# Optimization experiments

Hardware: AMD Instinct MI355X
Metric: run time of the kernel (lower is better)

Reference implementation:

```python
import jax, jax.numpy as jnp
import numpy as np

EPS = 1e-5


def conv2d(x, w, b, pad, mode='reflect'):
    # x: [B,C,H,W], w: [O,I,kh,kw]
    if pad > 0:
        x = jnp.pad(x, ((0, 0), (0, 0), (pad, pad), (pad, pad)), mode=mode)
    y = jax.lax.conv_general_dilated(x, w, (1, 1), 'VALID',
                                     dimension_numbers=('NCHW', 'OIHW', 'NCHW'))
    return y + b[None, :, None, None]


def inorm(x):
    # InstanceNorm2d, no affine (nn.InstanceNorm2d default)
    m = jnp.mean(x, axis=(2, 3), keepdims=True)
    v = jnp.mean((x - m) ** 2, axis=(2, 3), keepdims=True)
    return (x - m) * jax.lax.rsqrt(v + EPS)


def upsample2(x):
    # nn.Upsample(scale_factor=2), default nearest
    return jnp.repeat(jnp.repeat(x, 2, axis=2), 2, axis=3)


def bilinear_sample(img, py, px):
    # img [B,C,H,W]; py/px [B,H,W] float coords; zero padding outside bounds
    B, C, H, W = img.shape
    y0 = jnp.floor(py)
    x0 = jnp.floor(px)
    wy1 = (py - y0)[:, None]
    wx1 = (px - x0)[:, None]
    wy0 = 1.0 - wy1
    wx0 = 1.0 - wx1
    y0i = y0.astype(jnp.int32)
    x0i = x0.astype(jnp.int32)
    flat = img.reshape(B, C, H * W)

    def tap(yi, xi):
        valid = (yi >= 0) & (yi < H) & (xi >= 0) & (xi < W)
        idx = jnp.clip(yi, 0, H - 1) * W + jnp.clip(xi, 0, W - 1)
        g = jnp.take_along_axis(flat, idx.reshape(B, 1, H * W), axis=2).reshape(B, C, H, W)
        return g * valid[:, None]

    return (tap(y0i, x0i) * wy0 * wx0 + tap(y0i, x0i + 1) * wy0 * wx1 +
            tap(y0i + 1, x0i) * wy1 * wx0 + tap(y0i + 1, x0i + 1) * wy1 * wx1)


def mdcn(x, offset, mask, w, b):
    # modulated deformable conv v2: 3x3, stride 1, pad 1, 1 deformable group
    # offset [B,18,H,W] read as interleaved (dy,dx) per kernel tap; mask [B,9,H,W]
    B, C, H, W = x.shape
    off = offset.reshape(B, 9, 2, H, W)
    base_y = jnp.arange(H, dtype=x.dtype)[None, :, None]
    base_x = jnp.arange(W, dtype=x.dtype)[None, None, :]
    cols = []
    for k in range(9):
        ky, kx = k // 3 - 1, k % 3 - 1
        py = base_y + ky + off[:, k, 0]
        px = base_x + kx + off[:, k, 1]
        cols.append(bilinear_sample(x, py, px) * mask[:, k][:, None])
    col = jnp.stack(cols, axis=2)  # [B,C,9,H,W]
    out = jnp.einsum('bckhw,ock->bohw', col, w.reshape(w.shape[0], C, 9))
    return out + b[None, :, None, None]


def dcn_block(out, skip, off_w, off_b, w, b):
    # ModulatedDeformConvPack(double=True): offsets from concat, deform conv on skip
    dc = jnp.concatenate([out, skip], axis=1)
    om = conv2d(dc, off_w, off_b, 1, mode='constant')
    o1, o2, m = jnp.split(om, 3, axis=1)
    offset = jnp.concatenate([o1, o2], axis=1)
    pre = mdcn(skip, offset, jax.nn.sigmoid(m), w, b)
    return jnp.concatenate([pre, out], axis=1), offset


def decoder_fwd(x, skip1, skip2,
                rb0_w1, rb0_b1, rb0_w2, rb0_b2,
                rb1_w1, rb1_b1, rb1_w2, rb1_b2,
                conv1_w, conv1_b, conv3_w, conv3_b,
                conv5_w, conv5_b, conv6_w, conv6_b,
                dcn2_off_w, dcn2_off_b, dcn2_w, dcn2_b,
                dcn1_off_w, dcn1_off_b, dcn1_w, dcn1_b):
    out = x
    # i=0: ResBlocks (2 resblocks, 'in' norm, relu, reflect pad)
    for (w1, b1, w2, b2) in ((rb0_w1, rb0_b1, rb0_w2, rb0_b2),
                             (rb1_w1, rb1_b1, rb1_w2, rb1_b2)):
        h = jax.nn.relu(inorm(conv2d(out, w1, b1, 1)))
        out = out + inorm(conv2d(h, w2, b2, 1))
    # i=1: Conv2dBlock(256->256, 5x5)
    out = jax.nn.relu(inorm(conv2d(out, conv1_w, conv1_b, 2)))
    # dcn_2 hook (baseline_idx=2 -> dcn_idx=[1,3])
    out, offset2 = dcn_block(out, skip2, dcn2_off_w, dcn2_off_b, dcn2_w, dcn2_b)
    # i=2: upsample
    out = upsample2(out)
    # i=3: Conv2dBlock(512->128, 5x5)
    out = jax.nn.relu(inorm(conv2d(out, conv3_w, conv3_b, 2)))
    # dcn hook
    out, offset1 = dcn_block(out, skip1, dcn1_off_w, dcn1_off_b, dcn1_w, dcn1_b)
    # i=4: upsample
    out = upsample2(out)
    # i=5: Conv2dBlock(256->64, 5x5)
    out = jax.nn.relu(inorm(conv2d(out, conv5_w, conv5_b, 2)))
    # i=6: Conv2dBlock(64->3, 7x7, no norm, tanh)
    out = jnp.tanh(conv2d(out, conv6_w, conv6_b, 3))
    offset_sum = 0.5 * (jnp.mean(jnp.abs(offset1)) + jnp.mean(jnp.abs(offset2)))
    return out, offset_sum


def setup_inputs() -> dict:
    key = jax.random.key(0)
    ks = iter(jax.random.split(key, 48))

    def randn(shape, scale=1.0):
        return jax.random.normal(next(ks), shape, dtype=jnp.float32) * scale

    def conv_w(o, i, k, scale=1.0):
        return randn((o, i, k, k), scale / float(np.sqrt(i * k * k)))

    d = {}
    d['x'] = randn((8, 256, 32, 32))
    d['skip1'] = randn((8, 128, 64, 64))
    d['skip2'] = randn((8, 256, 32, 32))
    for r in range(2):
        d[f'rb{r}_w1'] = conv_w(256, 256, 3)
        d[f'rb{r}_b1'] = randn((256,), 0.01)
        d[f'rb{r}_w2'] = conv_w(256, 256, 3)
        d[f'rb{r}_b2'] = randn((256,), 0.01)
    d['conv1_w'] = conv_w(256, 256, 5); d['conv1_b'] = randn((256,), 0.01)
    d['conv3_w'] = conv_w(128, 512, 5); d['conv3_b'] = randn((128,), 0.01)
    d['conv5_w'] = conv_w(64, 256, 5); d['conv5_b'] = randn((64,), 0.01)
    d['conv6_w'] = conv_w(3, 64, 7); d['conv6_b'] = randn((3,), 0.01)
    d['dcn2_off_w'] = conv_w(27, 512, 3, 0.1); d['dcn2_off_b'] = randn((27,), 0.01)
    d['dcn2_w'] = conv_w(256, 256, 3); d['dcn2_b'] = randn((256,), 0.01)
    d['dcn1_off_w'] = conv_w(27, 256, 3, 0.1); d['dcn1_off_b'] = randn((27,), 0.01)
    d['dcn1_w'] = conv_w(128, 128, 3); d['dcn1_b'] = randn((128,), 0.01)
    return d


def reference(x, skip1, skip2,
              rb0_w1, rb0_b1, rb0_w2, rb0_b2,
              rb1_w1, rb1_b1, rb1_w2, rb1_b2,
              conv1_w, conv1_b, conv3_w, conv3_b,
              conv5_w, conv5_b, conv6_w, conv6_b,
              dcn2_off_w, dcn2_off_b, dcn2_w, dcn2_b,
              dcn1_off_w, dcn1_off_b, dcn1_w, dcn1_b):
    return decoder_fwd(x, skip1, skip2,
                       rb0_w1, rb0_b1, rb0_w2, rb0_b2,
                       rb1_w1, rb1_b1, rb1_w2, rb1_b2,
                       conv1_w, conv1_b, conv3_w, conv3_b,
                       conv5_w, conv5_b, conv6_w, conv6_b,
                       dcn2_off_w, dcn2_off_b, dcn2_w, dcn2_b,
                       dcn1_off_w, dcn1_off_b, dcn1_w, dcn1_b)
```

## Files before the change

kernel.cpp:

```cpp
#include <hip/hip_runtime.h>
#include <hip/hip_bf16.h>
#include <math.h>

typedef __hip_bfloat16 bf16;
typedef unsigned short u16;
typedef __attribute__((ext_vector_type(8))) short short8;
typedef __attribute__((ext_vector_type(4))) float f32x4;

__device__ __forceinline__ float LD(const float* p) { return *p; }
__device__ __forceinline__ float LD(const bf16* p)  { return __bfloat162float(*p); }
__device__ __forceinline__ void  ST(float* p, float v) { *p = v; }
__device__ __forceinline__ void  ST(bf16* p, float v)  { *p = __float2bfloat16(v); }
__device__ __forceinline__ u16   f2b(float v) { bf16 h = __float2bfloat16(v); return *reinterpret_cast<u16*>(&h); }
__device__ __forceinline__ float b2fu(u16 u) { bf16 h = *reinterpret_cast<bf16*>(&u); return __bfloat162float(h); }

__global__ __launch_bounds__(256) void copy_kernel(const float* __restrict__ in,
                                                   float* __restrict__ out, int n) {
    int i = blockIdx.x * blockDim.x + threadIdx.x;
    if (i < n) out[i] = in[i];
}

__global__ __launch_bounds__(256) void wsplit_kernel(const float* __restrict__ w,
                                                     u16* __restrict__ hi, u16* __restrict__ lo,
                                                     int O, int C, int KK)
{
    const int i = blockIdx.x * 256 + threadIdx.x;
    const int n = O * C * KK;
    if (i >= n) return;
    const int o = i / (C * KK);
    const int r = i - o * C * KK;
    const int c = r / KK;
    const int t = r - c * KK;
    const float v = w[i];
    const bf16 h = __float2bfloat16(v);
    const float hv = __bfloat162float(h);
    const bf16 l = __float2bfloat16(v - hv);
    const size_t dst = ((size_t)t * O + o) * C + c;
    hi[dst] = *(const u16*)&h;
    lo[dst] = *(const u16*)&l;
}

__global__ __launch_bounds__(256) void wsplit2_kernel(const float* __restrict__ w,
                                                      u16* __restrict__ hi, u16* __restrict__ lo,
                                                      int O, int C, int KK)
{
    const int i = blockIdx.x * 256 + threadIdx.x;
    const int n = O * C * KK;
    if (i >= n) return;
    const int o = i / (C * KK);
    const int r = i - o * C * KK;
    const int c = r / KK;
    const int t = r - c * KK;
    const float v = w[i];
    const bf16 h = __float2bfloat16(v);
    const float hv = __bfloat162float(h);
    const bf16 l = __float2bfloat16(v - hv);
    const int nch = C >> 5;
    const int cc = c >> 5, quad = (c >> 3) & 3, q = c & 7;
    const size_t dst = ((((size_t)t * nch + cc) * 4 + quad) * O + o) * 8 + q;
    hi[dst] = *(const u16*)&h;
    lo[dst] = *(const u16*)&l;
}

__global__ __launch_bounds__(256) void wsplitL_kernel(const float* __restrict__ w,
        u16* __restrict__ lh, u16* __restrict__ ll, u16* __restrict__ ch, int O, int C)
{
    const int i = blockIdx.x * 256 + threadIdx.x;
    const int n = O * C * 50;
    if (i >= n) return;
    const int s = i / (O * C);
    const int r = i - s * (O * C);
    const int o = r / C;
    const int c = r - o * C;
    const size_t U = (size_t)C * O;
    const int cc = c >> 5, quad = (c >> 3) & 3, q = c & 7;
    const size_t din = (((size_t)cc * 4 + quad) * O + o) * 8 + q;
    const float* wp = w + ((size_t)o * C + c) * 25;
    if (s < 30) {
        const int ry = s / 15, rem = s % 15, j = rem / 5, tx = rem % 5;
        int ys, yn;
        if (ry == 0) { ys = (j == 0) ? 0 : (j == 1) ? 2 : 4; yn = (j == 2) ? 1 : 2; }
        else         { ys = (j == 0) ? 0 : (j == 1) ? 1 : 3; yn = (j == 0) ? 1 : 2; }
        float v = 0.f;
        for (int ty = ys; ty < ys + yn; ++ty) v += wp[ty * 5 + tx];
        const bf16 h = __float2bfloat16(v);
        const bf16 l = __float2bfloat16(v - __bfloat162float(h));
        lh[(size_t)s * U + din] = *(const u16*)&h;
        ll[(size_t)s * U + din] = *(const u16*)&l;
    } else {
        const int t = s - 30;
        const int cidx = t / 5, tx = t - cidx * 5;
        const int tyc = (cidx == 0) ? 0 : (cidx == 1) ? 1 : (cidx == 2) ? 3 : 4;
        const bf16 h = __float2bfloat16(wp[tyc * 5 + tx]);
        ch[(size_t)t * U + din] = *(const u16*)&h;
    }
}

template<typename T1, typename T2, int K, bool UP, int EPI, bool ASPLIT,
         int NR, int NCOL, int MT, int MW>
__global__ __launch_bounds__(MW * 128) void conv_mfma3(
        const T1* __restrict__ src1, const T2* __restrict__ src2,
        int C1, int C,
        const u16* __restrict__ wth, const u16* __restrict__ wtl,
        const float* __restrict__ bias,
        void* __restrict__ outv, int O, int H, int W)
{
    constexpr int KK = K * K;
    constexpr int ATILE = NR * NCOL * 32;
    __shared__ __align__(16) u16 Ah[ATILE];
    __shared__ __align__(16) u16 Al[ASPLIT ? ATILE : 8];

    const int tid  = threadIdx.x;
    const int lane = tid & 63;
    const int wv   = tid >> 6;
    const int ln15 = lane & 15;
    const int quad = lane >> 4;
    const int mi = wv % MW, ni = wv / MW;
    const int b = blockIdx.y;
    const int p0 = blockIdx.x * (MT * 16 * MW);
    const int obase = blockIdx.z * 64;
    const int HW = H * W;
    const int SH = UP ? (H >> 1) : H;
    const int SW = UP ? (W >> 1) : W;
    const int SHW = SH * SW;
    const int PAD = K / 2;
    const int C2 = C - C1;
    const int nch = C >> 5;

    const int y0 = p0 / W;
    const int rbase = (y0 <= PAD) ? 0 : (UP ? ((y0 - PAD) >> 1) : (y0 - PAD));

    int rs[MT][K], cs[MT][K];
#pragma unroll
    for (int ms = 0; ms < MT; ++ms) {
        const int pm = p0 + mi * (MT * 16) + ms * 16 + ln15;
        const int ym = pm / W, xm = pm - ym * W;
#pragma unroll
        for (int tt = 0; tt < K; ++tt) {
            int yy = ym + tt - PAD;
            yy = yy < 0 ? -yy : yy; yy = yy >= H ? 2 * H - 2 - yy : yy;
            rs[ms][tt] = (UP ? (yy >> 1) : yy) - rbase;
            int xx = xm + tt - PAD;
            xx = xx < 0 ? -xx : xx; xx = xx >= W ? 2 * W - 2 - xx : xx;
            cs[ms][tt] = UP ? (xx >> 1) : xx;
        }
    }

    f32x4 acc[MT][2];
#pragma unroll
    for (int i = 0; i < MT; ++i)
#pragma unroll
        for (int j = 0; j < 2; ++j) acc[i][j] = (f32x4)0.f;

    for (int cc = 0; cc < nch; ++cc) {
        const int c0 = cc << 5;
        __syncthreads();
        for (int idx = tid; idx < NR * NCOL * 4; idx += MW * 128) {
            const int c_ = idx % NCOL;
            const int r_ = (idx / NCOL) % NR;
            const int cq = idx / (NCOL * NR);
            int rr = rbase + r_; rr = rr >= SH ? SH - 1 : rr;
            const int sidx = rr * SW + c_;
            short8 vh, vl;
#pragma unroll
            for (int q = 0; q < 8; ++q) {
                const int c = c0 + cq * 8 + q;
                float v;
                if (c < C1) v = LD(src1 + (size_t)(b * C1 + c) * SHW + sidx);
                else        v = LD(src2 + (size_t)(b * C2 + (c - C1)) * SHW + sidx);
                const u16 hv = f2b(v);
                vh[q] = (short)hv;
                if (ASPLIT) vl[q] = (short)f2b(v - b2fu(hv));
            }
            *(short8*)&Ah[idx * 8] = vh;
            if (ASPLIT) *(short8*)&Al[idx * 8] = vl;
        }
        __syncthreads();

#pragma unroll
        for (int t = 0; t < KK; ++t) {
            const int ty = t / K, tx = t - ty * K;
            const size_t wb0 = ((((size_t)t * nch + cc) * 4 + quad) * O
                                + obase + ni * 32 + ln15) * 8;
            const short8 b0h = *(const short8*)(wth + wb0);
            const short8 b1h = *(const short8*)(wth + wb0 + 128);
            const short8 b0l = *(const short8*)(wtl + wb0);
            const short8 b1l = *(const short8*)(wtl + wb0 + 128);
#pragma unroll
            for (int ms = 0; ms < MT; ++ms) {
                const int ao = ((quad * NR + rs[ms][ty]) * NCOL + cs[ms][tx]) * 8;
                const short8 a = *(const short8*)&Ah[ao];
                acc[ms][0] = __builtin_amdgcn_mfma_f32_16x16x32_bf16(a, b0h, acc[ms][0], 0, 0, 0);
                acc[ms][0] = __builtin_amdgcn_mfma_f32_16x16x32_bf16(a, b0l, acc[ms][0], 0, 0, 0);
                acc[ms][1] = __builtin_amdgcn_mfma_f32_16x16x32_bf16(a, b1h, acc[ms][1], 0, 0, 0);
                acc[ms][1] = __builtin_amdgcn_mfma_f32_16x16x32_bf16(a, b1l, acc[ms][1], 0, 0, 0);
                if (ASPLIT) {
                    const short8 al = *(const short8*)&Al[ao];
                    acc[ms][0] = __builtin_amdgcn_mfma_f32_16x16x32_bf16(al, b0h, acc[ms][0], 0, 0, 0);
                    acc[ms][1] = __builtin_amdgcn_mfma_f32_16x16x32_bf16(al, b1h, acc[ms][1], 0, 0, 0);
                }
            }
        }
    }

#pragma unroll
    for (int ms = 0; ms < MT; ++ms) {
#pragma unroll
        for (int ns = 0; ns < 2; ++ns) {
            const int o = obase + ni * 32 + ns * 16 + ln15;
            const float bv = bias[o];
            const f32x4 av = acc[ms][ns];
#pragma unroll
            for (int r = 0; r < 4; ++r) {
                const int pp = p0 + mi * (MT * 16) + ms * 16 + (quad << 2) + r;
                const float v = av[r] + bv;
                const size_t oidx = ((size_t)(b * O + o)) * HW + pp;
                if (EPI == 0) ((float*)outv)[oidx] = v;
                else          ((bf16*)outv)[oidx] = __float2bfloat16(v);
            }
        }
    }
}

template<typename T1, typename T2, int NR, int NCOL, int MT, int MW>
__global__ __launch_bounds__(MW * 128) void conv_mfma5(
        const T1* __restrict__ src1, const T2* __restrict__ src2,
        int C1, int C,
        const u16* __restrict__ wLh, const u16* __restrict__ wLl,
        const u16* __restrict__ wCh,
        const float* __restrict__ bias,
        bf16* __restrict__ out, int O, int H, int W)
{
    constexpr int NRR = NR + 1;
    __shared__ __align__(16) u16 Ah[4 * NRR * NCOL * 8];

    const int tid  = threadIdx.x;
    const int lane = tid & 63;
    const int wv   = tid >> 6;
    const int ln15 = lane & 15;
    const int quad = lane >> 4;
    const int mi = wv % MW, ni = wv / MW;
    const int b = blockIdx.y;
    const int p0 = blockIdx.x * (MT * 16 * MW);
    const int obase = blockIdx.z * 64;
    const int HW = H * W;
    const int SH = H >> 1, SW = W >> 1;
    const int SHW = SH * SW;
    const int C2 = C - C1;
    const int nch = C >> 5;
    const size_t U = (size_t)C * O;

    const int y0 = p0 / W;
    const int rbase = (y0 <= 2) ? 0 : ((y0 - 2) >> 1);

    const int ym0 = (p0 + mi * (MT * 16)) / W;
    const int ry = ym0 & 1;
    const int uu = ym0 >> 1;
    int r0 = uu - 1, r2 = uu + 1;
    r0 = r0 < 0 ? 1 : r0;
    r2 = r2 >= SH ? SH - 2 : r2;
    const int rg0 = r0 - rbase, rg1 = uu - rbase, rg2 = r2 - rbase;

    const bool isTopW = (ym0 <= 1), isBotW = (ym0 >= H - 2);
    const bool isBorderW = isTopW || isBotW;
    int cidx = 0;
    if (isTopW) cidx = (ym0 == 0) ? 1 : 0;
    if (isBotW) cidx = (ym0 == H - 2) ? 3 : 2;
    const bool blkTop = (p0 == 0);
    const bool blkBot = (p0 + MW * MT * 16 == HW);
    const bool blkEdge = blkTop || blkBot;

    int cs[MT][5];
#pragma unroll
    for (int ms = 0; ms < MT; ++ms) {
        const int pm = p0 + mi * (MT * 16) + ms * 16 + ln15;
        const int xm = pm % W;
#pragma unroll
        for (int tt = 0; tt < 5; ++tt) {
            int xx = xm + tt - 2;
            xx = xx < 0 ? -xx : xx; xx = xx >= W ? 2 * W - 2 - xx : xx;
            cs[ms][tt] = xx >> 1;
        }
    }

    f32x4 acc[MT][2];
#pragma unroll
    for (int i = 0; i < MT; ++i)
#pragma unroll
        for (int j = 0; j < 2; ++j) acc[i][j] = (f32x4)0.f;

    for (int cc = 0; cc < nch; ++cc) {
        const int c0 = cc << 5;
        __syncthreads();
        for (int idx = tid; idx < NR * NCOL * 4; idx += MW * 128) {
            const int c_ = idx % NCOL;
            const int r_ = (idx / NCOL) % NR;
            const int cq = idx / (NCOL * NR);
            int rr = rbase + r_; rr = rr >= SH ? SH - 1 : rr;
            const int sidx = rr * SW + c_;
            short8 vh;
#pragma unroll
            for (int q = 0; q < 8; ++q) {
                const int c = c0 + cq * 8 + q;
                float v;
                if (c < C1) v = LD(src1 + (size_t)(b * C1 + c) * SHW + sidx);
                else        v = LD(src2 + (size_t)(b * C2 + (c - C1)) * SHW + sidx);
                vh[q] = (short)f2b(v);
            }
            *(short8*)&Ah[((cq * NRR + r_) * NCOL + c_) * 8] = vh;
        }
        if (blkEdge) {
            const int ra = blkTop ? 0 : SH - 1;
            const int rb2 = blkTop ? 1 : SH - 2;
            for (int idx = tid; idx < NCOL * 4; idx += MW * 128) {
                const int c_ = idx % NCOL;
                const int cq = idx / NCOL;
                short8 vh;
#pragma unroll
                for (int q = 0; q < 8; ++q) {
                    const int c = c0 + cq * 8 + q;
                    float va, vb;
                    if (c < C1) {
                        const size_t base = (size_t)(b * C1 + c) * SHW;
                        va = LD(src1 + base + ra * SW + c_);
                        vb = LD(src1 + base + rb2 * SW + c_);
                    } else {
                        const size_t base = (size_t)(b * C2 + (c - C1)) * SHW;
                        va = LD(src2 + base + ra * SW + c_);
                        vb = LD(src2 + base + rb2 * SW + c_);
                    }
                    vh[q] = (short)f2b(va - vb);
                }
                *(short8*)&Ah[((cq * NRR + NR) * NCOL + c_) * 8] = vh;
            }
        }
        __syncthreads();

        const size_t wq = ((size_t)(cc * 4 + quad) * O + obase + ni * 32 + ln15) * 8;
#pragma unroll
        for (int j = 0; j < 3; ++j) {
            const int rgj = (j == 0) ? rg0 : (j == 1) ? rg1 : rg2;
#pragma unroll
            for (int tx = 0; tx < 5; ++tx) {
                const size_t wb = (size_t)((ry * 3 + j) * 5 + tx) * U + wq;
                const short8 b0h = *(const short8*)(wLh + wb);
                const short8 b1h = *(const short8*)(wLh + wb + 128);
                const short8 b0l = *(const short8*)(wLl + wb);
                const short8 b1l = *(const short8*)(wLl + wb + 128);
#pragma unroll
                for (int ms = 0; ms < MT; ++ms) {
                    const int ao = ((quad * NRR + rgj) * NCOL + cs[ms][tx]) * 8;
                    const short8 a = *(const short8*)&Ah[ao];
                    acc[ms][0] = __builtin_amdgcn_mfma_f32_16x16x32_bf16(a, b0h, acc[ms][0], 0, 0, 0);
                    acc[ms][0] = __builtin_amdgcn_mfma_f32_16x16x32_bf16(a, b0l, acc[ms][0], 0, 0, 0);
                    acc[ms][1] = __builtin_amdgcn_mfma_f32_16x16x32_bf16(a, b1h, acc[ms][1], 0, 0, 0);
                    acc[ms][1] = __builtin_amdgcn_mfma_f32_16x16x32_bf16(a, b1l, acc[ms][1], 0, 0, 0);
                }
            }
        }
        if (isBorderW) {
#pragma unroll
            for (int tx = 0; tx < 5; ++tx) {
                const size_t wb = (size_t)(cidx * 5 + tx) * U + wq;
                const short8 b0 = *(const short8*)(wCh + wb);
                const short8 b1 = *(const short8*)(wCh + wb + 128);
#pragma unroll
                for (int ms = 0; ms < MT; ++ms) {
                    const int ao = ((quad * NRR + NR) * NCOL + cs[ms][tx]) * 8;
                    const short8 a = *(const short8*)&Ah[ao];
                    acc[ms][0] = __builtin_amdgcn_mfma_f32_16x16x32_bf16(a, b0, acc[ms][0], 0, 0, 0);
                    acc[ms][1] = __builtin_amdgcn_mfma_f32_16x16x32_bf16(a, b1, acc[ms][1], 0, 0, 0);
                }
            }
        }
    }

#pragma unroll
    for (int ms = 0; ms < MT; ++ms) {
#pragma unroll
        for (int ns = 0; ns < 2; ++ns) {
            const int o = obase + ni * 32 + ns * 16 + ln15;
            const float bv = bias[o];
            const f32x4 av = acc[ms][ns];
#pragma unroll
            for (int r = 0; r < 4; ++r) {
                const int pp = p0 + mi * (MT * 16) + ms * 16 + (quad << 2) + r;
                out[((size_t)(b * O + o)) * HW + pp] = __float2bfloat16(av[r] + bv);
            }
        }
    }
}

template<typename OT, bool ASPLIT>
__global__ __launch_bounds__(256) void mdcn_mfma(
        const float* __restrict__ skip, const float* __restrict__ om,
        const u16* __restrict__ wth, const u16* __restrict__ wtl,
        const float* __restrict__ bias,
        OT* __restrict__ out, int C, int O, int H, int W)
{
    __shared__ float tpy[576], tpxs[576], tms[576];
    __shared__ __align__(16) u16 Ah[2][2048];
    __shared__ __align__(16) u16 Al[ASPLIT ? 2 : 1][2048];
    __shared__ __align__(16) u16 Bs[2][2][2048];

    const int tid = threadIdx.x;
    const int lane = tid & 63;
    const int wv = tid >> 6;
    const int ln15 = lane & 15;
    const int quad = lane >> 4;
    const int mi = wv & 1, ni = wv >> 1;
    const int flat = blockIdx.x + gridDim.x * (blockIdx.y + 8 * blockIdx.z);
    const int b = flat & 7;
    const int rest = flat >> 3;
    const int p0 = (rest % gridDim.x) * 64;
    const int obase = (rest / gridDim.x) * 64;
    const int HW = H * W;
    const int nch = C >> 5;

    const float* omb = om + (size_t)b * 27 * HW;
    for (int i = tid; i < 576; i += 256) {
        const int k = i >> 6, px_ = i & 63;
        const int p = p0 + px_;
        const int y = p / W, x = p - y * W;
        const float dy = omb[(2 * k) * HW + p];
        const float dx = omb[(2 * k + 1) * HW + p];
        const float mk = 1.f / (1.f + expf(-omb[(18 + k) * HW + p]));
        float py = (float)(y + k / 3 - 1) + dy;
        float pxx = (float)(x + k % 3 - 1) + dx;
        py  = fminf(fmaxf(py, -2.f), (float)H + 1.f);
        pxx = fminf(fmaxf(pxx, -2.f), (float)W + 1.f);
        tpy[i] = py; tpxs[i] = pxx; tms[i] = mk;
    }
    __syncthreads();

    f32x4 acc[2][2];
#pragma unroll
    for (int i = 0; i < 2; ++i)
#pragma unroll
        for (int j = 0; j < 2; ++j) acc[i][j] = (f32x4)0.f;

    const float* xb = skip + (size_t)b * C * HW;
    const int swA = (lane >> 1) & 3;
    const int awr = (lane * 4 + (wv ^ swA)) * 8;
    const int pix0 = mi * 32 + ln15;
    const int pix1 = pix0 + 16;
    const int ao0 = (pix0 * 4 + (quad ^ ((pix0 >> 1) & 3))) * 8;
    const int ao1 = (pix1 * 4 + (quad ^ ((pix1 >> 1) & 3))) * 8;
    const int bo0 = (quad * 64 + ni * 32 + ln15) * 8;
    const int bo1 = bo0 + 16 * 8;

    int chunk = 0;
    for (int cc = 0; cc < nch; ++cc) {
        const int c0c = cc << 5;
        const float* pb = xb + (size_t)(c0c + (wv << 3)) * HW;
        for (int k = 0; k < 9; ++k, ++chunk) {
            const int s = chunk & 1;
            const float py = tpy[k * 64 + lane], pxx = tpxs[k * 64 + lane], mk = tms[k * 64 + lane];
            const float y0f = floorf(py), x0f = floorf(pxx);
            const int y0 = (int)y0f, x0 = (int)x0f;
            const float wy1 = py - y0f, wx1 = pxx - x0f;
            const float wy0 = 1.f - wy1, wx0 = 1.f - wx1;
            const bool r0v = (y0 >= 0 && y0 < H), r1v = (y0 + 1 >= 0 && y0 + 1 < H);
            const bool c0v = (x0 >= 0 && x0 < W), c1v = (x0 + 1 >= 0 && x0 + 1 < W);
            const float w00 = (r0v && c0v) ? wy0 * wx0 * mk : 0.f;
            const float w01 = (r0v && c1v) ? wy0 * wx1 * mk : 0.f;
            const float w10 = (r1v && c0v) ? wy1 * wx0 * mk : 0.f;
            const float w11 = (r1v && c1v) ? wy1 * wx1 * mk : 0.f;
            const int i00 = (r0v ? y0 : 0) * W + (c0v ? x0 : 0);
            const int i01 = (r0v ? y0 : 0) * W + (c1v ? x0 + 1 : 0);
            const int i10 = (r1v ? y0 + 1 : 0) * W + (c0v ? x0 : 0);
            const int i11 = (r1v ? y0 + 1 : 0) * W + (c1v ? x0 + 1 : 0);
            {
                short8 vh, vl;
#pragma unroll
                for (int q = 0; q < 8; ++q) {
                    const float* pl = pb + (size_t)q * HW;
                    const float v = w00 * pl[i00] + w01 * pl[i01] + w10 * pl[i10] + w11 * pl[i11];
                    const u16 hv = f2b(v);
                    vh[q] = (short)hv;
                    if (ASPLIT) vl[q] = (short)f2b(v - b2fu(hv));
                }
                *(short8*)&Ah[s][awr] = vh;
                if (ASPLIT) *(short8*)&Al[s][awr] = vl;
            }
            {
                const size_t base = ((((size_t)k * nch + cc) * 4 + wv) * O + obase + lane) * 8;
                *(short8*)&Bs[s][0][tid * 8] = *(const short8*)(wth + base);
                *(short8*)&Bs[s][1][tid * 8] = *(const short8*)(wtl + base);
            }
            __syncthreads();
            const short8 a0 = *(const short8*)&Ah[s][ao0];
            const short8 a1 = *(const short8*)&Ah[s][ao1];
            const short8 b0h = *(const short8*)&Bs[s][0][bo0];
            const short8 b1h = *(const short8*)&Bs[s][0][bo1];
            const short8 b0l = *(const short8*)&Bs[s][1][bo0];
            const short8 b1l = *(const short8*)&Bs[s][1][bo1];
            acc[0][0] = __builtin_amdgcn_mfma_f32_16x16x32_bf16(a0, b0h, acc[0][0], 0, 0, 0);
            acc[0][0] = __builtin_amdgcn_mfma_f32_16x16x32_bf16(a0, b0l, acc[0][0], 0, 0, 0);
            acc[0][1] = __builtin_amdgcn_mfma_f32_16x16x32_bf16(a0, b1h, acc[0][1], 0, 0, 0);
            acc[0][1] = __builtin_amdgcn_mfma_f32_16x16x32_bf16(a0, b1l, acc[0][1], 0, 0, 0);
            acc[1][0] = __builtin_amdgcn_mfma_f32_16x16x32_bf16(a1, b0h, acc[1][0], 0, 0, 0);
            acc[1][0] = __builtin_amdgcn_mfma_f32_16x16x32_bf16(a1, b0l, acc[1][0], 0, 0, 0);
            acc[1][1] = __builtin_amdgcn_mfma_f32_16x16x32_bf16(a1, b1h, acc[1][1], 0, 0, 0);
            acc[1][1] = __builtin_amdgcn_mfma_f32_16x16x32_bf16(a1, b1l, acc[1][1], 0, 0, 0);
            if (ASPLIT) {
                const short8 a0l = *(const short8*)&Al[s][ao0];
                const short8 a1l = *(const short8*)&Al[s][ao1];
                acc[0][0] = __builtin_amdgcn_mfma_f32_16x16x32_bf16(a0l, b0h, acc[0][0], 0, 0, 0);
                acc[0][1] = __builtin_amdgcn_mfma_f32_16x16x32_bf16(a0l, b1h, acc[0][1], 0, 0, 0);
                acc[1][0] = __builtin_amdgcn_mfma_f32_16x16x32_bf16(a1l, b0h, acc[1][0], 0, 0, 0);
                acc[1][1] = __builtin_amdgcn_mfma_f32_16x16x32_bf16(a1l, b1h, acc[1][1], 0, 0, 0);
            }
        }
    }

#pragma unroll
    for (int ms = 0; ms < 2; ++ms) {
#pragma unroll
        for (int ns = 0; ns < 2; ++ns) {
            const int o = obase + ni * 32 + ns * 16 + ln15;
            const float bv = bias[o];
#pragma unroll
            for (int r = 0; r < 4; ++r) {
                const int pp = p0 + mi * 32 + ms * 16 + (quad << 2) + r;
                ST(out + ((size_t)(b * O + o)) * HW + pp, acc[ms][ns][r] + bv);
            }
        }
    }
}

template<typename T1, typename T2, int K, bool REFLECT, bool UP, int NTN, int EPI, bool ASPLIT>
__global__ __launch_bounds__(256) void conv_mfma(
        const T1* __restrict__ src1, const T2* __restrict__ src2,
        int C1, int C,
        const u16* __restrict__ wth, const u16* __restrict__ wtl,
        const float* __restrict__ bias,
        void* __restrict__ outv, int O, int H, int W)
{
    constexpr int KK = K * K;
    __shared__ __align__(16) u16 As[64 * 40];
    __shared__ __align__(16) u16 Alo[ASPLIT ? 64 * 40 : 8];
    __shared__ __align__(16) u16 Bh[NTN * 16 * 40];
    __shared__ __align__(16) u16 Bl[NTN * 16 * 40];

    const int tid  = threadIdx.x;
    const int wv   = tid >> 6;
    const int lane = tid & 63;
    const int ln15 = lane & 15;
    const int b    = blockIdx.y;
    const int p0   = blockIdx.x * 64;
    const int obase = blockIdx.z * (NTN * 16);
    const int HW = H * W;
    const int Hs = UP ? (H >> 1) : H;
    const int Ws = UP ? (W >> 1) : W;
    const int HsWs = Hs * Ws;
    const int PAD = K / 2;
    const int C2 = C - C1;
    const int m_stage = tid & 63;

    const int p = p0 + m_stage;
    const int y = p / W, x = p - y * W;
    int off[KK];
    float msk[KK];
#pragma unroll
    for (int ty = 0; ty < K; ++ty) {
#pragma unroll
        for (int tx = 0; tx < K; ++tx) {
            int yy = y + ty - PAD, xx = x + tx - PAD;
            bool vv = true;
            if (REFLECT) {
                yy = yy < 0 ? -yy : yy; yy = yy >= H ? 2 * H - 2 - yy : yy;
                xx = xx < 0 ? -xx : xx; xx = xx >= W ? 2 * W - 2 - xx : xx;
            } else {
                vv = (yy >= 0 && yy < H && xx >= 0 && xx < W);
                yy = yy < 0 ? 0 : (yy >= H ? H - 1 : yy);
                xx = xx < 0 ? 0 : (xx >= W ? W - 1 : xx);
            }
            off[ty * K + tx] = (UP ? (yy >> 1) : yy) * Ws + (UP ? (xx >> 1) : xx);
            msk[ty * K + tx] = vv ? 1.f : 0.f;
        }
    }

    f32x4 acc[NTN];
#pragma unroll
    for (int nt = 0; nt < NTN; ++nt) acc[nt] = (f32x4)0.f;

    const int aswz = (m_stage >> 3) & 3;
    const int awr  = m_stage * 40 + ((wv ^ aswz) << 3);
    const int arow = wv * 16 + ln15;
    const int ard  = arow * 40 + (((lane >> 4) ^ ((arow >> 3) & 3)) << 3);

    const int nch = C >> 5;
    for (int cc = 0; cc < nch; ++cc) {
        const int c0 = cc << 5;
        for (int t = 0; t < KK; ++t) {
            const int offt = off[t];
            const float mskt = msk[t];
            __syncthreads();
            {
                short8 avh, avl;
#pragma unroll
                for (int q = 0; q < 8; ++q) {
                    const int c = c0 + (wv << 3) + q;
                    float v;
                    if (c < C1) v = LD(src1 + ((size_t)(b * C1 + c)) * HsWs + offt);
                    else        v = LD(src2 + ((size_t)(b * C2 + (c - C1))) * HsWs + offt);
                    if (!REFLECT) v *= mskt;
                    const u16 hv = f2b(v);
                    avh[q] = (short)hv;
                    if (ASPLIT) avl[q] = (short)f2b(v - b2fu(hv));
                }
                *(short8*)&As[awr] = avh;
                if (ASPLIT) *(short8*)&Alo[awr] = avl;
            }
            for (int i = tid; i < NTN * 16 * 4; i += 256) {
                const int row = i >> 2, part = i & 3;
                int o = obase + row; if (o >= O) o = O - 1;
                const int pw = row * 40 + ((part ^ ((row >> 3) & 3)) << 3);
                const size_t wb = ((size_t)t * O + o) * C + c0 + (part << 3);
                *(short8*)&Bh[pw] = *(const short8*)(wth + wb);
                *(short8*)&Bl[pw] = *(const short8*)(wtl + wb);
            }
            __syncthreads();
            const short8 a = *(const short8*)&As[ard];
            short8 al;
            if (ASPLIT) al = *(const short8*)&Alo[ard];
#pragma unroll
            for (int nt = 0; nt < NTN; ++nt) {
                const int brow = nt * 16 + ln15;
                const int brd = brow * 40 + (((lane >> 4) ^ ((brow >> 3) & 3)) << 3);
                const short8 bh = *(const short8*)&Bh[brd];
                acc[nt] = __builtin_amdgcn_mfma_f32_16x16x32_bf16(a, bh, acc[nt], 0, 0, 0);
                const short8 bl = *(const short8*)&Bl[brd];
                acc[nt] = __builtin_amdgcn_mfma_f32_16x16x32_bf16(a, bl, acc[nt], 0, 0, 0);
                if (ASPLIT)
                    acc[nt] = __builtin_amdgcn_mfma_f32_16x16x32_bf16(al, bh, acc[nt], 0, 0, 0);
            }
        }
    }

#pragma unroll
    for (int nt = 0; nt < NTN; ++nt) {
        const int o = obase + nt * 16 + ln15;
        if (o < O) {
            const float bv = bias[o];
#pragma unroll
            for (int r = 0; r < 4; ++r) {
                const int pp = p0 + wv * 16 + ((lane >> 4) << 2) + r;
                const float v = acc[nt][r] + bv;
                const size_t oidx = ((size_t)(b * O + o)) * HW + pp;
                if (EPI == 0)      ((float*)outv)[oidx] = v;
                else if (EPI == 1) ((float*)outv)[oidx] = tanhf(v);
                else               ((bf16*)outv)[oidx] = __float2bfloat16(v);
            }
        }
    }
}

template<typename T>
__global__ __launch_bounds__(256) void inorm_kernel(T* __restrict__ buf,
                                                    float* __restrict__ resid,
                                                    int HW, int mode)
{
    __shared__ double sh0[256], sh1[256];
    const int pl = blockIdx.x;
    T* p = buf + (size_t)pl * HW;
    double s = 0.0, ss = 0.0;
    for (int i = threadIdx.x; i < HW; i += 256) {
        float v = LD(p + i);
        s += (double)v; ss += (double)v * (double)v;
    }
    sh0[threadIdx.x] = s; sh1[threadIdx.x] = ss;
    __syncthreads();
    for (int st = 128; st > 0; st >>= 1) {
        if (threadIdx.x < st) {
            sh0[threadIdx.x] += sh0[threadIdx.x + st];
            sh1[threadIdx.x] += sh1[threadIdx.x + st];
        }
        __syncthreads();
    }
    const double mean = sh0[0] / HW;
    const float m = (float)mean;
    const float var = (float)(sh1[0] / HW - mean * mean);
    const float inv = rsqrtf(var + 1e-5f);
    if (mode == 0) {
        for (int i = threadIdx.x; i < HW; i += 256) {
            float v = (LD(p + i) - m) * inv;
            ST(p + i, v > 0.f ? v : 0.f);
        }
    } else {
        float* r = resid + (size_t)pl * HW;
        for (int i = threadIdx.x; i < HW; i += 256)
            r[i] = r[i] + (LD(p + i) - m) * inv;
    }
}

__global__ void zero1_kernel(float* __restrict__ out) { if (threadIdx.x == 0) out[0] = 0.f; }

__global__ __launch_bounds__(256) void offsum_one(const float* __restrict__ om, int HW,
                                                  float* __restrict__ out)
{
    __shared__ double sh[256];
    const int n = 8 * 18 * HW;
    double s = 0.0;
    for (int i = blockIdx.x * 256 + threadIdx.x; i < n; i += gridDim.x * 256) {
        const int b = i / (18 * HW); const int r = i - b * 18 * HW;
        const int c = r / HW; const int p = r - c * HW;
        s += fabs((double)om[(size_t)(b * 27 + c) * HW + p]);
    }
    sh[threadIdx.x] = s;
    __syncthreads();
    for (int st = 128; st > 0; st >>= 1) {
        if (threadIdx.x < st) sh[threadIdx.x] += sh[threadIdx.x + st];
        __syncthreads();
    }
    if (threadIdx.x == 0) atomicAdd(out, (float)(0.5 * sh[0] / n));
}

extern "C" void kernel_launch(void* const* d_in, const int* in_sizes, int n_in,
                              void* d_out, int out_size, void* d_ws, size_t ws_size,
                              hipStream_t stream)
{
    if (n_in < 27) return;
    if (out_size < 393217) return;
    if (in_sizes[0] != 8 * 256 * 32 * 32) return;
    if (in_sizes[1] != 8 * 128 * 64 * 64) return;
    if (in_sizes[2] != 8 * 256 * 32 * 32) return;
    if (in_sizes[25] != 128 * 128 * 9) return;
    if (in_sizes[26] != 128) return;

    const float* x        = (const float*)d_in[0];
    const float* skip1    = (const float*)d_in[1];
    const float* skip2    = (const float*)d_in[2];
    const float* rbw[2][2] = {{(const float*)d_in[3], (const float*)d_in[5]},
                              {(const float*)d_in[7], (const float*)d_in[9]}};
    const float* rbb[2][2] = {{(const float*)d_in[4], (const float*)d_in[6]},
                              {(const float*)d_in[8], (const float*)d_in[10]}};
    const float* conv1_w = (const float*)d_in[11]; const float* conv1_b = (const float*)d_in[12];
    const float* conv3_w = (const float*)d_in[13]; const float* conv3_b = (const float*)d_in[14];
    const float* conv5_w = (const float*)d_in[15]; const float* conv5_b = (const float*)d_in[16];
    const float* conv6_w = (const float*)d_in[17]; const float* conv6_b = (const float*)d_in[18];
    const float* dcn2_off_w = (const float*)d_in[19]; const float* dcn2_off_b = (const float*)d_in[20];
    const float* dcn2_w = (const float*)d_in[21]; const float* dcn2_b = (const float*)d_in[22];
    const float* dcn1_off_w = (const float*)d_in[23]; const float* dcn1_off_b = (const float*)d_in[24];
    const float* dcn1_w = (const float*)d_in[25]; const float* dcn1_b = (const float*)d_in[26];

    float* outp = (float*)d_out;

    const size_t NEED_F32 = 9494528ull;
    if (ws_size < NEED_F32 * 4ull) return;

    float* ws = (float*)d_ws;
    const size_t NA = 2097152ull;
    float* A   = ws;
    float* Bb  = ws + NA;
    float* Tmp = ws + 2 * NA;
    float* om2 = ws + 3 * NA;
    float* om1 = om2 + 221184;
    bf16*  Fb  = (bf16*)(om1 + 884736);
    bf16*  Ib  = (bf16*)A;
    bf16*  Jb  = (bf16*)Bb;
    u16*   wm2h = (u16*)Tmp;
    u16*   wm2l = wm2h + 589824;
    u16*   wo2h = (u16*)(Tmp + 589824);
    u16*   wo2l = wo2h + 124416;
    u16*   wL3h = (u16*)Tmp;
    u16*   wL3l = wL3h + 30 * 65536;
    u16*   wC3h = wL3l + 30 * 65536;
    u16*   wo1h = (u16*)Tmp;
    u16*   wo1l = wo1h + 62208;
    u16*   wm1h = (u16*)Bb;
    u16*   wm1l = wm1h + 147456;
    u16*   wL5h = (u16*)om1;
    u16*   wL5l = wL5h + 30 * 16384;
    u16*   wC5h = wL5l + 30 * 16384;
    u16*   wt6h = (u16*)om2;
    u16*   wt6l = wt6h + 9408;
    u16*   wEh = (u16*)Fb;

    copy_kernel<<<8192, 256, 0, stream>>>(x, A, (int)NA);

    for (int r = 0; r < 2; ++r) {
        wsplit2_kernel<<<2304, 256, 0, stream>>>(rbw[r][0], wEh, wEh + 589824, 256, 256, 9);
        conv_mfma3<float, float, 3, false, 0, true, 4, 32, 2, 2><<<dim3(16, 8, 4), 256, 0, stream>>>(
            A, (const float*)nullptr, 256, 256, wEh, wEh + 589824, rbb[r][0], Bb, 256, 32, 32);
        inorm_kernel<float><<<2048, 256, 0, stream>>>(Bb, nullptr, 1024, 0);
        wsplit2_kernel<<<2304, 256, 0, stream>>>(rbw[r][1], wEh, wEh + 589824, 256, 256, 9);
        conv_mfma3<float, float, 3, false, 0, true, 4, 32, 2, 2><<<dim3(16, 8, 4), 256, 0, stream>>>(
            Bb, (const float*)nullptr, 256, 256, wEh, wEh + 589824, rbb[r][1], Tmp, 256, 32, 32);
        inorm_kernel<float><<<2048, 256, 0, stream>>>(Tmp, A, 1024, 1);
    }

    wsplit2_kernel<<<6400, 256, 0, stream>>>(conv1_w, wEh, wEh + 1638400, 256, 256, 25);
    conv_mfma3<float, float, 5, false, 0, true, 6, 32, 2, 2><<<dim3(16, 8, 4), 256, 0, stream>>>(
        A, (const float*)nullptr, 256, 256, wEh, wEh + 1638400, conv1_b, Bb, 256, 32, 32);
    inorm_kernel<float><<<2048, 256, 0, stream>>>(Bb, nullptr, 1024, 0);

    wsplit_kernel<<<486, 256, 0, stream>>>(dcn2_off_w, wo2h, wo2l, 27, 512, 9);
    conv_mfma<float, float, 3, false, false, 2, 0, false><<<dim3(16, 8, 1), 256, 0, stream>>>(
        Bb, skip2, 256, 512, wo2h, wo2l, dcn2_off_b, om2, 27, 32, 32);
    wsplit2_kernel<<<2304, 256, 0, stream>>>(dcn2_w, wm2h, wm2l, 256, 256, 9);
    mdcn_mfma<float, true><<<dim3(16, 8, 4), 256, 0, stream>>>(
        skip2, om2, wm2h, wm2l, dcn2_b, A, 256, 256, 32, 32);

    zero1_kernel<<<1, 64, 0, stream>>>(outp + 393216);
    offsum_one<<<64, 256, 0, stream>>>(om2, 1024, outp + 393216);

    wsplitL_kernel<<<12800, 256, 0, stream>>>(conv3_w, wL3h, wL3l, wC3h, 128, 512);
    conv_mfma5<float, float, 4, 32, 4, 4><<<dim3(16, 8, 2), 512, 0, stream>>>(
        A, Bb, 256, 512, wL3h, wL3l, wC3h, conv3_b, Fb, 128, 64, 64);
    inorm_kernel<bf16><<<1024, 256, 0, stream>>>(Fb, nullptr, 4096, 0);

    wsplit_kernel<<<243, 256, 0, stream>>>(dcn1_off_w, wo1h, wo1l, 27, 256, 9);
    conv_mfma<bf16, float, 3, false, false, 2, 0, false><<<dim3(64, 8, 1), 256, 0, stream>>>(
        Fb, skip1, 128, 256, wo1h, wo1l, dcn1_off_b, om1, 27, 64, 64);
    wsplit2_kernel<<<576, 256, 0, stream>>>(dcn1_w, wm1h, wm1l, 128, 128, 9);
    mdcn_mfma<bf16, true><<<dim3(64, 8, 2), 256, 0, stream>>>(
        skip1, om1, wm1h, wm1l, dcn1_b, Ib, 128, 128, 64, 64);

    offsum_one<<<64, 256, 0, stream>>>(om1, 4096, outp + 393216);

    wsplitL_kernel<<<3200, 256, 0, stream>>>(conv5_w, wL5h, wL5l, wC5h, 64, 256);
    conv_mfma5<bf16, bf16, 3, 64, 4, 4><<<dim3(64, 8, 1), 512, 0, stream>>>(
        Ib, Fb, 128, 256, wL5h, wL5l, wC5h, conv5_b, Jb, 64, 128, 128);
    inorm_kernel<bf16><<<512, 256, 0, stream>>>(Jb, nullptr, 16384, 0);

    wsplit_kernel<<<37, 256, 0, stream>>>(conv6_w, wt6h, wt6l, 3, 64, 49);
    conv_mfma<bf16, float, 7, true, false, 1, 1, false><<<dim3(256, 8, 1), 256, 0, stream>>>(
        Jb, (const float*)nullptr, 64, 64, wt6h, wt6l, conv6_b, (void*)outp, 3, 128, 128);
}
```

Baseline: 1.546 ms.

## Split-K the dcn2 deformable conv across channel halves with atomic accumulation

The 32x32 dcn2 deformable conv now splits its input-channel loop into two halves, doubling the grid (z from 4 to 8), and accumulates partial results into a pre-zeroed output with float atomicAdd. Only the first half adds the bias. The bilinear gather loop is also restructured to issue all 32 corner loads before the weighted sums, to expose memory-level parallelism. This adds an extra zeroing kernel and atomic traffic in exchange for more blocks on the small layer, and it makes the summation order nondeterministic.

```diff
diff --git a/kernel.cpp b/kernel.cpp
--- a/kernel.cpp
+++ b/kernel.cpp
@@ -18,6 +18,11 @@
                                                    float* __restrict__ out, int n) {
     int i = blockIdx.x * blockDim.x + threadIdx.x;
     if (i < n) out[i] = in[i];
+}
+
+__global__ __launch_bounds__(256) void zero_kernel(float* __restrict__ p, int n) {
+    int i = blockIdx.x * blockDim.x + threadIdx.x;
+    if (i < n) p[i] = 0.f;
 }
 
 __global__ __launch_bounds__(256) void wsplit_kernel(const float* __restrict__ w,
@@ -391,7 +396,7 @@
     }
 }
 
-template<typename OT, bool ASPLIT>
+template<typename OT, bool ASPLIT, bool KS>
 __global__ __launch_bounds__(256) void mdcn_mfma(
         const float* __restrict__ skip, const float* __restrict__ om,
         const u16* __restrict__ wth, const u16* __restrict__ wtl,
@@ -413,9 +418,14 @@
     const int b = flat & 7;
     const int rest = flat >> 3;
     const int p0 = (rest % gridDim.x) * 64;
-    const int obase = (rest / gridDim.x) * 64;
+    int oz = rest / gridDim.x;
+    int khalf = 0;
+    if (KS) { khalf = oz >> 2; oz &= 3; }
+    const int obase = oz * 64;
     const int HW = H * W;
     const int nch = C >> 5;
+    const int ccs = KS ? khalf * (nch >> 1) : 0;
+    const int cce = KS ? ccs + (nch >> 1) : nch;
 
     const float* omb = om + (size_t)b * 27 * HW;
     for (int i = tid; i < 576; i += 256) {
@@ -450,7 +460,7 @@
     const int bo1 = bo0 + 16 * 8;
 
     int chunk = 0;
-    for (int cc = 0; cc < nch; ++cc) {
+    for (int cc = ccs; cc < cce; ++cc) {
         const int c0c = cc << 5;
         const float* pb = xb + (size_t)(c0c + (wv << 3)) * HW;
         for (int k = 0; k < 9; ++k, ++chunk) {
@@ -471,11 +481,19 @@
             const int i10 = (r1v ? y0 + 1 : 0) * W + (c0v ? x0 : 0);
             const int i11 = (r1v ? y0 + 1 : 0) * W + (c1v ? x0 + 1 : 0);
             {
-                short8 vh, vl;
+                float t00[8], t01[8], t10[8], t11[8];
 #pragma unroll
                 for (int q = 0; q < 8; ++q) {
                     const float* pl = pb + (size_t)q * HW;
-                    const float v = w00 * pl[i00] + w01 * pl[i01] + w10 * pl[i10] + w11 * pl[i11];
+                    t00[q] = pl[i00];
+                    t01[q] = pl[i01];
+                    t10[q] = pl[i10];
+                    t11[q] = pl[i11];
+                }
+                short8 vh, vl;
+#pragma unroll
+                for (int q = 0; q < 8; ++q) {
+                    const float v = w00 * t00[q] + w01 * t01[q] + w10 * t10[q] + w11 * t11[q];
                     const u16 hv = f2b(v);
                     vh[q] = (short)hv;
                     if (ASPLIT) vl[q] = (short)f2b(v - b2fu(hv));
@@ -519,11 +537,16 @@
 #pragma unroll
         for (int ns = 0; ns < 2; ++ns) {
             const int o = obase + ni * 32 + ns * 16 + ln15;
-            const float bv = bias[o];
+            const float bv = (!KS || khalf == 0) ? bias[o] : 0.f;
 #pragma unroll
             for (int r = 0; r < 4; ++r) {
                 const int pp = p0 + mi * 32 + ms * 16 + (quad << 2) + r;
-                ST(out + ((size_t)(b * O + o)) * HW + pp, acc[ms][ns][r] + bv);
+                const size_t oi = ((size_t)(b * O + o)) * HW + pp;
+                if constexpr (KS) {
+                    atomicAdd((float*)out + oi, acc[ms][ns][r] + bv);
+                } else {
+                    ST(out + oi, acc[ms][ns][r] + bv);
+                }
             }
         }
     }
@@ -800,7 +823,8 @@
     conv_mfma<float, float, 3, false, false, 2, 0, false><<<dim3(16, 8, 1), 256, 0, stream>>>(
         Bb, skip2, 256, 512, wo2h, wo2l, dcn2_off_b, om2, 27, 32, 32);
     wsplit2_kernel<<<2304, 256, 0, stream>>>(dcn2_w, wm2h, wm2l, 256, 256, 9);
-    mdcn_mfma<float, true><<<dim3(16, 8, 4), 256, 0, stream>>>(
+    zero_kernel<<<8192, 256, 0, stream>>>(A, (int)NA);
+    mdcn_mfma<float, true, true><<<dim3(16, 8, 8), 256, 0, stream>>>(
         skip2, om2, wm2h, wm2l, dcn2_b, A, 256, 256, 32, 32);
 
     zero1_kernel<<<1, 64, 0, stream>>>(outp + 393216);
@@ -815,7 +839,7 @@
     conv_mfma<bf16, float, 3, false, false, 2, 0, false><<<dim3(64, 8, 1), 256, 0, stream>>>(
         Fb, skip1, 128, 256, wo1h, wo1l, dcn1_off_b, om1, 27, 64, 64);
     wsplit2_kernel<<<576, 256, 0, stream>>>(dcn1_w, wm1h, wm1l, 128, 128, 9);
-    mdcn_mfma<bf16, true><<<dim3(64, 8, 2), 256, 0, stream>>>(
+    mdcn_mfma<bf16, true, false><<<dim3(64, 8, 2), 256, 0, stream>>>(
         skip1, om1, wm1h, wm1l, dcn1_b, Ib, 128, 128, 64, 64);
 
     offsum_one<<<64, 256, 0, stream>>>(om1, 4096, outp + 393216);
```

Result: no change. 1.560 ms (+0.9%).

## Gather deformable-conv inputs from NHWC bf16 hi/lo split copies

Applied to the files above, without the earlier changes.

Adds a transpose kernel that converts the skip tensors from NCHW fp32 into NHWC bf16 hi/lo pairs. The deformable conv then gathers each bilinear tap as one contiguous 8-channel vector load instead of eight strided scalar loads. Workspace buffers are reassigned to hold the new copies. The cost is an extra transpose pass per DCN, twice as many load streams (hi and lo), and a small precision change from reconstructing inputs as the sum of two bf16 values.

```diff
diff --git a/kernel.cpp b/kernel.cpp
--- a/kernel.cpp
+++ b/kernel.cpp
@@ -18,6 +18,31 @@
                                                    float* __restrict__ out, int n) {
     int i = blockIdx.x * blockDim.x + threadIdx.x;
     if (i < n) out[i] = in[i];
+}
+
+__global__ __launch_bounds__(256) void nhwc_split_kernel(const float* __restrict__ in,
+                                                         u16* __restrict__ hi, u16* __restrict__ lo,
+                                                         int C, int HW)
+{
+    __shared__ float tile[32][65];
+    const int b = blockIdx.z;
+    const int c0 = blockIdx.y * 32;
+    const int p0 = blockIdx.x * 64;
+    for (int i = threadIdx.x; i < 2048; i += 256) {
+        const int c_ = i >> 6, p_ = i & 63;
+        tile[c_][p_] = in[((size_t)(b * C + c0 + c_)) * HW + p0 + p_];
+    }
+    __syncthreads();
+    for (int i = threadIdx.x; i < 2048; i += 256) {
+        const int p_ = i >> 5, c_ = i & 31;
+        const float v = tile[c_][p_];
+        const bf16 h = __float2bfloat16(v);
+        const float hv = __bfloat162float(h);
+        const bf16 l = __float2bfloat16(v - hv);
+        const size_t dst = ((size_t)b * HW + p0 + p_) * C + c0 + c_;
+        hi[dst] = *(const u16*)&h;
+        lo[dst] = *(const u16*)&l;
+    }
 }
 
 __global__ __launch_bounds__(256) void wsplit_kernel(const float* __restrict__ w,
@@ -393,7 +418,8 @@
 
 template<typename OT, bool ASPLIT>
 __global__ __launch_bounds__(256) void mdcn_mfma(
-        const float* __restrict__ skip, const float* __restrict__ om,
+        const u16* __restrict__ skiph, const u16* __restrict__ skipl,
+        const float* __restrict__ om,
         const u16* __restrict__ wth, const u16* __restrict__ wtl,
         const float* __restrict__ bias,
         OT* __restrict__ out, int C, int O, int H, int W)
@@ -439,7 +465,8 @@
 #pragma unroll
         for (int j = 0; j < 2; ++j) acc[i][j] = (f32x4)0.f;
 
-    const float* xb = skip + (size_t)b * C * HW;
+    const u16* xbh = skiph + (size_t)b * HW * C;
+    const u16* xbl = skipl + (size_t)b * HW * C;
     const int swA = (lane >> 1) & 3;
     const int awr = (lane * 4 + (wv ^ swA)) * 8;
     const int pix0 = mi * 32 + ln15;
@@ -451,8 +478,7 @@
 
     int chunk = 0;
     for (int cc = 0; cc < nch; ++cc) {
-        const int c0c = cc << 5;
-        const float* pb = xb + (size_t)(c0c + (wv << 3)) * HW;
+        const int cbase = (cc << 5) + (wv << 3);
         for (int k = 0; k < 9; ++k, ++chunk) {
             const int s = chunk & 1;
             const float py = tpy[k * 64 + lane], pxx = tpxs[k * 64 + lane], mk = tms[k * 64 + lane];
@@ -471,11 +497,22 @@
             const int i10 = (r1v ? y0 + 1 : 0) * W + (c0v ? x0 : 0);
             const int i11 = (r1v ? y0 + 1 : 0) * W + (c1v ? x0 + 1 : 0);
             {
+                const short8 h00 = *(const short8*)(xbh + (size_t)i00 * C + cbase);
+                const short8 h01 = *(const short8*)(xbh + (size_t)i01 * C + cbase);
+                const short8 h10 = *(const short8*)(xbh + (size_t)i10 * C + cbase);
+                const short8 h11 = *(const short8*)(xbh + (size_t)i11 * C + cbase);
+                const short8 l00 = *(const short8*)(xbl + (size_t)i00 * C + cbase);
+                const short8 l01 = *(const short8*)(xbl + (size_t)i01 * C + cbase);
+                const short8 l10 = *(const short8*)(xbl + (size_t)i10 * C + cbase);
+                const short8 l11 = *(const short8*)(xbl + (size_t)i11 * C + cbase);
                 short8 vh, vl;
 #pragma unroll
                 for (int q = 0; q < 8; ++q) {
-                    const float* pl = pb + (size_t)q * HW;
-                    const float v = w00 * pl[i00] + w01 * pl[i01] + w10 * pl[i10] + w11 * pl[i11];
+                    const float x00 = b2fu((u16)h00[q]) + b2fu((u16)l00[q]);
+                    const float x01 = b2fu((u16)h01[q]) + b2fu((u16)l01[q]);
+                    const float x10 = b2fu((u16)h10[q]) + b2fu((u16)l10[q]);
+                    const float x11 = b2fu((u16)h11[q]) + b2fu((u16)l11[q]);
+                    const float v = w00 * x00 + w01 * x01 + w10 * x10 + w11 * x11;
                     const u16 hv = f2b(v);
                     vh[q] = (short)hv;
                     if (ASPLIT) vl[q] = (short)f2b(v - b2fu(hv));
@@ -767,16 +804,20 @@
     u16*   wL3h = (u16*)Tmp;
     u16*   wL3l = wL3h + 30 * 65536;
     u16*   wC3h = wL3l + 30 * 65536;
-    u16*   wo1h = (u16*)Tmp;
+    u16*   wm1h = (u16*)om2;
+    u16*   wm1l = wm1h + 147456;
+    u16*   wo1h = wm1h + 294912;
     u16*   wo1l = wo1h + 62208;
-    u16*   wm1h = (u16*)Bb;
-    u16*   wm1l = wm1h + 147456;
     u16*   wL5h = (u16*)om1;
     u16*   wL5l = wL5h + 30 * 16384;
     u16*   wC5h = wL5l + 30 * 16384;
     u16*   wt6h = (u16*)om2;
     u16*   wt6l = wt6h + 9408;
     u16*   wEh = (u16*)Fb;
+    u16*   s2h = (u16*)Fb;
+    u16*   s2l = s2h + 2097152;
+    u16*   s1h = (u16*)Bb;
+    u16*   s1l = (u16*)Tmp;
 
     copy_kernel<<<8192, 256, 0, stream>>>(x, A, (int)NA);
 
@@ -796,12 +837,14 @@
         A, (const float*)nullptr, 256, 256, wEh, wEh + 1638400, conv1_b, Bb, 256, 32, 32);
     inorm_kernel<float><<<2048, 256, 0, stream>>>(Bb, nullptr, 1024, 0);
 
+    nhwc_split_kernel<<<dim3(16, 8, 8), 256, 0, stream>>>(skip2, s2h, s2l, 256, 1024);
+
     wsplit_kernel<<<486, 256, 0, stream>>>(dcn2_off_w, wo2h, wo2l, 27, 512, 9);
     conv_mfma<float, float, 3, false, false, 2, 0, false><<<dim3(16, 8, 1), 256, 0, stream>>>(
         Bb, skip2, 256, 512, wo2h, wo2l, dcn2_off_b, om2, 27, 32, 32);
     wsplit2_kernel<<<2304, 256, 0, stream>>>(dcn2_w, wm2h, wm2l, 256, 256, 9);
     mdcn_mfma<float, true><<<dim3(16, 8, 4), 256, 0, stream>>>(
-        skip2, om2, wm2h, wm2l, dcn2_b, A, 256, 256, 32, 32);
+        s2h, s2l, om2, wm2h, wm2l, dcn2_b, A, 256, 256, 32, 32);
 
     zero1_kernel<<<1, 64, 0, stream>>>(outp + 393216);
     offsum_one<<<64, 256, 0, stream>>>(om2, 1024, outp + 393216);
@@ -815,8 +858,9 @@
     conv_mfma<bf16, float, 3, false, false, 2, 0, false><<<dim3(64, 8, 1), 256, 0, stream>>>(
         Fb, skip1, 128, 256, wo1h, wo1l, dcn1_off_b, om1, 27, 64, 64);
     wsplit2_kernel<<<576, 256, 0, stream>>>(dcn1_w, wm1h, wm1l, 128, 128, 9);
+    nhwc_split_kernel<<<dim3(64, 4, 8), 256, 0, stream>>>(skip1, s1h, s1l, 128, 4096);
     mdcn_mfma<bf16, true><<<dim3(64, 8, 2), 256, 0, stream>>>(
-        skip1, om1, wm1h, wm1l, dcn1_b, Ib, 128, 128, 64, 64);
+        s1h, s1l, om1, wm1h, wm1l, dcn1_b, Ib, 128, 128, 64, 64);
 
     offsum_one<<<64, 256, 0, stream>>>(om1, 4096, outp + 393216);
 
```

New measurement: 1.466 ms. 1.05x faster.
